# Performance work log

Measured on AMD Instinct MI355X. Metric: run time of the kernel, lower is better.

## Reference

```python
import jax, jax.numpy as jnp
import numpy as np

CODEBOOK_SIZE = 1024
LATENT_DIM = 64
BETA = 0.25      # commitment_beta
DECAY = 0.99     # ema_decay
EPS = 1e-5       # ema_eps
DIVERSITY_W = 1.0


def _hadamard(n):
    # Sylvester construction (n must be a power of 2)
    H = np.array([[1.0]], dtype=np.float32)
    while H.shape[0] < n:
        H = np.block([[H, H], [H, -H]])
    return H.astype(np.float32)


def setup_inputs() -> dict:
    key = jax.random.key(0)
    k1, k2, k3 = jax.random.split(key, 3)
    B, C, H, W = 32, LATENT_DIM, 32, 32
    x = jax.random.normal(k1, (B, C, H, W), dtype=jnp.float32)
    embedding_weight = jax.random.normal(k2, (CODEBOOK_SIZE, LATENT_DIM), dtype=jnp.float32)
    rotation_matrix = jnp.asarray(_hadamard(LATENT_DIM))
    ema_w = jax.random.normal(k3, (CODEBOOK_SIZE, LATENT_DIM), dtype=jnp.float32)
    ema_cluster_size = jnp.ones((CODEBOOK_SIZE,), dtype=jnp.float32)
    return {"x": x, "embedding_weight": embedding_weight,
            "rotation_matrix": rotation_matrix, "ema_w": ema_w,
            "ema_cluster_size": ema_cluster_size}


def reference(x, embedding_weight, rotation_matrix, ema_w, ema_cluster_size):
    B, C, H, W = x.shape
    K, D = embedding_weight.shape
    N = B * H * W
    sg = jax.lax.stop_gradient

    # flatten channel-last, rotate
    xf = jnp.transpose(x, (0, 2, 3, 1)).reshape(N, D)      # [N, D]
    xr = xf @ rotation_matrix                               # [N, D]

    # pairwise squared distances to codebook + argmin
    dist = (jnp.sum(xr * xr, axis=-1, keepdims=True)
            + jnp.sum(embedding_weight * embedding_weight, axis=-1)[None, :]
            - 2.0 * (xr @ embedding_weight.T))              # [N, K]
    idx = jnp.argmin(dist, axis=-1)                         # [N]

    # one-hot scatter equivalents (counts / dw) done with index scatter-add
    counts = jnp.zeros((K,), x.dtype).at[idx].add(1.0)      # encodings.sum(0)
    quant = embedding_weight[idx]                           # [N, D]
    # NOTE: original code views (B*H*W, C) row-major directly as (B, C, H, W)
    quant_out = quant.reshape(B, C, H, W)

    # EMA codebook update (training=True path)
    cs = ema_cluster_size * DECAY + (1.0 - DECAY) * counts
    n = jnp.sum(cs)
    cs = (cs + EPS) / (n + K * EPS) * n
    dw = jnp.zeros((K, D), x.dtype).at[idx].add(xr)         # encodings.T @ xr
    new_ema_w = ema_w * DECAY + (1.0 - DECAY) * dw
    new_embedding = new_ema_w / cs[:, None]

    commitment_loss = BETA * jnp.mean((sg(quant_out) - x) ** 2)
    codebook_loss = jnp.mean((quant_out - sg(x)) ** 2)

    # diversity: mean over ALL (i, j) pairs of ||e_i - xr_j||^2 (original
    # broadcasts (N,1,D) vs (N,D) -> (N,N,D)); identical closed form:
    e = new_embedding[idx]                                  # [N, D]
    diversity_loss = DIVERSITY_W * (jnp.mean(jnp.sum(e * e, axis=-1))
                                    + jnp.mean(jnp.sum(xr * xr, axis=-1))
                                    - 2.0 * jnp.dot(jnp.mean(e, axis=0), jnp.mean(xr, axis=0)))

    avg_probs = counts / N
    perplexity = jnp.exp(-jnp.sum(avg_probs * jnp.log(avg_probs + 1e-10)))

    quant_st = x + sg(quant_out - x)                        # straight-through
    return (quant_st, codebook_loss, commitment_loss, diversity_loss,
            perplexity, idx, cs, new_ema_w, new_embedding)
```

## Files before the change

### kernel.cpp

```cpp
#include <hip/hip_runtime.h>
#include <math.h>

#define NTOK 32768
#define KCB  1024
#define DIM  64
#define THETA 0.02f

typedef __attribute__((ext_vector_type(8))) short short8;
typedef __attribute__((ext_vector_type(4))) float f32x4;
#define MFMA __builtin_amdgcn_mfma_f32_16x16x32_bf16
#define ALOAD(p) __hip_atomic_load((p), __ATOMIC_RELAXED, __HIP_MEMORY_SCOPE_AGENT)

#define WS_XR      0
#define WS_ENORM   2097152
#define WS_EH      2098176
#define WS_EL      2130944
#define WS_COUNTS  2163712
#define WS_CS      2164736
#define WS_XRSUM   2165760
#define WS_ESUM    2166272
#define WS_SCALREP 2166784
#define WS_FLAGCNT 2166912
#define WS_IDX     2166928
#define WS_FLAG    2199696

#define O_Q    0
#define O_CB   2097152
#define O_CM   2097153
#define O_DV   2097154
#define O_PP   2097155
#define O_IDX  2097156
#define O_CS   2129924
#define O_EW   2130948
#define O_EMB  2196484

__device__ __forceinline__ void hilo(float v, unsigned &h, unsigned &l)
{
    unsigned b  = __float_as_uint(v);
    unsigned hb = (b + 0x7FFFu + ((b >> 16) & 1u)) & 0xFFFF0000u;
    float lof   = v - __uint_as_float(hb);
    unsigned lb = __float_as_uint(lof);
    l = (lb + 0x7FFFu + ((lb >> 16) & 1u)) >> 16;
    h = hb >> 16;
}

__global__ __launch_bounds__(256) void k_rotate_enorm(const float* __restrict__ x,
    const float* __restrict__ E, float* __restrict__ xr, float* __restrict__ enorm,
    unsigned short* __restrict__ eh, unsigned short* __restrict__ el,
    float* __restrict__ counts, int* __restrict__ flagc,
    float* __restrict__ e_sum, float* __restrict__ xr_sum,
    float* __restrict__ scalrep)
{
    int tid = threadIdx.x;
    if (blockIdx.x >= 512) {
        int b = (int)blockIdx.x - 512;
        counts[(b << 8) + tid] = 0.f;
        if (b == 0) {
            if (tid < 16) flagc[tid] = 0;
            if (tid < 128) scalrep[tid] = 0.f;
        } else if (b == 1) {
            e_sum[tid] = 0.f; e_sum[256 + tid] = 0.f;
        } else if (b == 2) {
            xr_sum[tid] = 0.f; xr_sum[256 + tid] = 0.f;
        }
        int k = (b << 8) + tid;
        const float* ep = E + ((size_t)k << 6);
        unsigned* ehw = (unsigned*)eh + (k << 5);
        unsigned* elw = (unsigned*)el + (k << 5);
        float s = 0.f;
        #pragma unroll
        for (int q = 0; q < 32; ++q) {
            float v0 = ep[2*q], v1 = ep[2*q+1];
            s = fmaf(v0, v0, s); s = fmaf(v1, v1, s);
            unsigned h0, l0, h1, l1;
            hilo(v0, h0, l0);
            hilo(v1, h1, l1);
            ehw[q] = h0 | (h1 << 16);
            elw[q] = l0 | (l1 << 16);
        }
        enorm[k] = s;
        return;
    }
    __shared__ float xt[64 * 65];
    int p  = blockIdx.x >> 4;
    int s0 = ((int)blockIdx.x & 15) << 6;

    {
        const float4* x4 = (const float4*)x;
        #pragma unroll
        for (int pass = 0; pass < 4; ++pass) {
            int q = (pass << 8) + tid;
            int c = q >> 4, col = (q & 15) << 2;
            float4 v = x4[(p << 14) + (c << 8) + (s0 >> 2) + (col >> 2)];
            float* dst = xt + c * 65 + col;
            dst[0] = v.x; dst[1] = v.y; dst[2] = v.z; dst[3] = v.w;
        }
    }
    __syncthreads();

    int lane = tid & 63, w = tid >> 6;
    #pragma unroll
    for (int i = 0; i < 4; ++i) {
        int sl = (w << 4) + (i << 2);
        const float* src = xt + lane * 65 + sl;
        float4 v = make_float4(src[0], src[1], src[2], src[3]);
        #pragma unroll
        for (int s = 1; s <= 32; s <<= 1) {
            float sgn = (lane & s) ? -1.f : 1.f;
            float ox = __shfl_xor(v.x, s);
            float oy = __shfl_xor(v.y, s);
            float oz = __shfl_xor(v.z, s);
            float ow = __shfl_xor(v.w, s);
            v.x = fmaf(sgn, v.x, ox);
            v.y = fmaf(sgn, v.y, oy);
            v.z = fmaf(sgn, v.z, oz);
            v.w = fmaf(sgn, v.w, ow);
        }
        int t0 = ((int)blockIdx.x << 6) + sl;
        float* dst = xr + ((size_t)t0 << 6) + lane;
        dst[0]   = v.x;
        dst[64]  = v.y;
        dst[128] = v.z;
        dst[192] = v.w;
    }
}

__global__ __launch_bounds__(256, 4) void k_argmin(const float* __restrict__ xr,
    const unsigned short* __restrict__ eh, const unsigned short* __restrict__ el,
    const float* __restrict__ enorm, int* __restrict__ idxw,
    float* __restrict__ out_idx, float* __restrict__ counts,
    int* __restrict__ flag)
{
    __shared__ uint4 ehs[1024];
    __shared__ uint4 els[1024];
    __shared__ float ens[128];
    __shared__ float m_b1[32], m_b2[32];
    __shared__ int   m_id[32];
    int tid = threadIdx.x;
    int lane = tid & 63, w = tid >> 6;
    int ts = w >> 1, kh = w & 1;
    int tx = lane & 15, gq = lane >> 4;
    int tokbase = ((int)blockIdx.x << 5) + (ts << 4);

    short8 ah0, al0, ah1, al1;
    {
        const float* xp = xr + ((size_t)(tokbase + tx) << 6) + (gq << 3);
        float4 xa = *(const float4*)(xp);
        float4 xb = *(const float4*)(xp + 4);
        float4 xc = *(const float4*)(xp + 32);
        float4 xd = *(const float4*)(xp + 36);
        float a0v[8] = {xa.x,xa.y,xa.z,xa.w,xb.x,xb.y,xb.z,xb.w};
        float a1v[8] = {xc.x,xc.y,xc.z,xc.w,xd.x,xd.y,xd.z,xd.w};
        #pragma unroll
        for (int j = 0; j < 8; ++j) {
            unsigned h, l;
            hilo(a0v[j], h, l);
            ah0[j] = (short)h; al0[j] = (short)l;
            hilo(a1v[j], h, l);
            ah1[j] = (short)h; al1[j] = (short)l;
        }
    }

    float b1[4], b2[4]; int idx[4];
    #pragma unroll
    for (int r = 0; r < 4; ++r) { b1[r] = 3.4e38f; b2[r] = 3.4e38f; idx[r] = 0; }

    int swz0 = gq ^ (tx & 7);
    int swz1 = (4 + gq) ^ (tx & 7);
    const f32x4 z4 = {0.f, 0.f, 0.f, 0.f};

    for (int ch = 0; ch < 8; ++ch) {
        int c0 = ch << 7;
        __syncthreads();
        {
            const uint4* ghs = (const uint4*)eh + ((size_t)c0 << 3);
            const uint4* gls = (const uint4*)el + ((size_t)c0 << 3);
            #pragma unroll
            for (int i = 0; i < 4; ++i) {
                int u = (i << 8) + tid;
                int rr = u >> 3, bb = u & 7;
                int bs = bb ^ (rr & 7);
                ehs[(rr << 3) + bs] = ghs[u];
                els[(rr << 3) + bs] = gls[u];
            }
            if (tid < 128) ens[tid] = enorm[c0 + tid];
        }
        __syncthreads();

        #pragma unroll
        for (int s = 0; s < 4; ++s) {
            int rbase = (kh << 6) + (s << 4) + tx;
            short8 bh0 = ((const short8*)ehs)[(rbase << 3) + swz0];
            short8 bh1 = ((const short8*)ehs)[(rbase << 3) + swz1];
            short8 bl0 = ((const short8*)els)[(rbase << 3) + swz0];
            short8 bl1 = ((const short8*)els)[(rbase << 3) + swz1];

            f32x4 a0 = MFMA(ah0, bh0, z4, 0, 0, 0);
            a0 = MFMA(ah0, bl0, a0, 0, 0, 0);
            a0 = MFMA(al0, bh0, a0, 0, 0, 0);
            f32x4 a1 = MFMA(ah1, bh1, z4, 0, 0, 0);
            a1 = MFMA(ah1, bl1, a1, 0, 0, 0);
            a1 = MFMA(al1, bh1, a1, 0, 0, 0);

            float en = ens[rbase];
            int kk = c0 + rbase;
            #pragma unroll
            for (int r = 0; r < 4; ++r) {
                float sv = fmaf(-2.f, a0[r], fmaf(-2.f, a1[r], en));
                float mx = fmaxf(sv, b1[r]);
                b2[r] = fminf(b2[r], mx);
                bool t = sv < b1[r];
                idx[r] = t ? kk : idx[r];
                b1[r] = fminf(b1[r], sv);
            }
        }
    }

    float v1f[4], v2f[4]; int idf[4];
    #pragma unroll
    for (int r = 0; r < 4; ++r) {
        float v1 = b1[r], v2 = b2[r]; int id = idx[r];
        #pragma unroll
        for (int m = 1; m <= 8; m <<= 1) {
            float o1 = __shfl_xor(v1, m);
            float o2 = __shfl_xor(v2, m);
            int   oi = __shfl_xor(id, m);
            float nb2 = fminf(fminf(v2, o2), fmaxf(v1, o1));
            bool t = (o1 < v1) || (o1 == v1 && oi < id);
            v1 = t ? o1 : v1;
            id = t ? oi : id;
            v2 = nb2;
        }
        v1f[r] = v1; v2f[r] = v2; idf[r] = id;
    }

    int tl = (ts << 4) + (gq << 2);
    if (kh == 1 && tx == 0) {
        #pragma unroll
        for (int r = 0; r < 4; ++r) {
            m_b1[tl + r] = v1f[r];
            m_b2[tl + r] = v2f[r];
            m_id[tl + r] = idf[r];
        }
    }
    __syncthreads();
    if (kh == 0 && tx == 0) {
        #pragma unroll
        for (int r = 0; r < 4; ++r) {
            float o1 = m_b1[tl + r], o2 = m_b2[tl + r];
            int   oi = m_id[tl + r];
            float v1 = v1f[r]; int id = idf[r];
            float b2m = fminf(fminf(v2f[r], o2), fmaxf(v1, o1));
            bool t = (o1 < v1) || (o1 == v1 && oi < id);
            float v1m = t ? o1 : v1;
            int   idm = t ? oi : id;
            int tok = tokbase + (gq << 2) + r;
            idxw[tok] = idm;
            out_idx[tok] = (float)idm;
            atomicAdd(&counts[idm], 1.f);
            flag[tok] = (b2m - v1m < THETA) ? 1 : 0;
        }
    }
}

__global__ __launch_bounds__(256) void k_fixupquant_ema(const float* __restrict__ x,
    const float* __restrict__ xr, const float* __restrict__ E,
    const float* __restrict__ enorm, const float* __restrict__ ecs,
    const int* __restrict__ flag, int* __restrict__ idxw,
    float* __restrict__ out_idx, float* __restrict__ counts,
    float* __restrict__ out_cs, float* __restrict__ csw,
    int* __restrict__ done_ctr, float* __restrict__ outq,
    float* __restrict__ scalrep)
{
    __shared__ int lidx[32];
    __shared__ unsigned fmask;
    __shared__ float wr[4], wn[4];
    int tid = threadIdx.x;
    int lane = tid & 63, w = tid >> 6;
    int n0 = (int)blockIdx.x << 5;

    int fl = 0;
    if (tid < 32) {
        lidx[tid] = idxw[n0 + tid];
        fl = flag[n0 + tid];
    }
    unsigned long long bal = __ballot(fl != 0);
    if (tid == 0) fmask = (unsigned)bal;
    __syncthreads();

    unsigned msk = fmask;
    int widx = 0;
    while (msk) {
        int src = __ffs(msk) - 1; msk &= msk - 1;
        if ((widx++ & 3) != w) continue;
        int tok = n0 + src;
        const float4* xp = (const float4*)(xr + ((size_t)tok << 6));
        float4 xa[16];
        #pragma unroll
        for (int q = 0; q < 16; ++q) xa[q] = xp[q];
        float best = 3.4e38f; int bidx = 0;
        for (int c = 0; c < 16; ++c) {
            int k = (c << 6) + lane;
            const float4* epp = (const float4*)(E + ((size_t)k << 6));
            float d = 0.f;
            #pragma unroll
            for (int q = 0; q < 16; ++q) {
                float4 e = epp[q];
                d = fmaf(xa[q].x, e.x, d);
                d = fmaf(xa[q].y, e.y, d);
                d = fmaf(xa[q].z, e.z, d);
                d = fmaf(xa[q].w, e.w, d);
            }
            float sv = fmaf(-2.f, d, enorm[k]);
            if (sv < best) { best = sv; bidx = k; }
        }
        #pragma unroll
        for (int m = 1; m <= 32; m <<= 1) {
            float ov = __shfl_xor(best, m);
            int   oi = __shfl_xor(bidx, m);
            if (ov < best || (ov == best && oi < bidx)) { best = ov; bidx = oi; }
        }
        if (lane == 0) {
            int old = lidx[src];
            if (old != bidx) {
                atomicAdd(&counts[old], -1.f);
                atomicAdd(&counts[bidx], 1.f);
                lidx[src] = bidx;
                idxw[tok] = bidx;
                out_idx[tok] = (float)bidx;
            }
        }
    }
    __syncthreads();

    int f40 = (int)blockIdx.x << 9;
    float sq = 0.f, xn = 0.f;
    #pragma unroll
    for (int it = 0; it < 2; ++it) {
        int q = (it << 8) + tid;
        int kk = lidx[q >> 4];
        int d4 = q & 15;
        float4 xv = ((const float4*)x)[f40 + q];
        float4 ev = ((const float4*)E)[(kk << 4) + d4];
        float dx = ev.x - xv.x, dy = ev.y - xv.y, dz = ev.z - xv.z, dw_ = ev.w - xv.w;
        ((float4*)outq)[f40 + q] = make_float4(xv.x + dx, xv.y + dy, xv.z + dz, xv.w + dw_);
        sq += dx*dx + dy*dy + dz*dz + dw_*dw_;
        xn += xv.x*xv.x + xv.y*xv.y + xv.z*xv.z + xv.w*xv.w;
    }
    #pragma unroll
    for (int m = 32; m >= 1; m >>= 1) { sq += __shfl_xor(sq, m); xn += __shfl_xor(xn, m); }
    if (lane == 0) { wr[w] = sq; wn[w] = xn; }
    __syncthreads();
    if (tid == 0) {
        int rep = ((int)blockIdx.x & 7) << 4;
        atomicAdd(&scalrep[rep + 0], wr[0] + wr[1] + wr[2] + wr[3]);
        atomicAdd(&scalrep[rep + 1], wn[0] + wn[1] + wn[2] + wn[3]);
    }

    __shared__ int ticket;
    __syncthreads();
    if (tid == 0) ticket = atomicAdd(done_ctr, 1);
    __syncthreads();
    if (ticket != 1023) return;

    __shared__ float wsum2[4];
    __shared__ float nss;
    float cs4[4];
    float csum = 0.f;
    #pragma unroll
    for (int j = 0; j < 4; ++j) {
        int kk = (tid << 2) + j;
        float c = ALOAD(&counts[kk]);
        float cs = ecs[kk] * 0.99f + 0.01f * c;
        cs4[j] = cs;
        csum += cs;
    }
    float v = csum;
    #pragma unroll
    for (int m = 32; m >= 1; m >>= 1) v += __shfl_xor(v, m);
    if (lane == 0) wsum2[w] = v;
    __syncthreads();
    if (tid == 0) nss = wsum2[0] + wsum2[1] + wsum2[2] + wsum2[3];
    __syncthreads();
    float nn = nss;
    #pragma unroll
    for (int j = 0; j < 4; ++j) {
        int kk = (tid << 2) + j;
        float csf = (cs4[j] + 1e-5f) / (nn + 1024.f * 1e-5f) * nn;
        out_cs[kk] = csf;
        csw[kk] = csf;
    }
}

__global__ __launch_bounds__(256) void k_dwemb_final(const float* __restrict__ xr,
    const int* __restrict__ idxw, const float* __restrict__ counts,
    const float* __restrict__ csw, const float* __restrict__ emaw,
    float* __restrict__ out_ew, float* __restrict__ out_emb,
    float* __restrict__ e_sum, float* __restrict__ scalrep,
    float* __restrict__ xr_sum, float* __restrict__ out,
    int* __restrict__ done_ctr)
{
    __shared__ float part[3][64];
    __shared__ int   lst[2048];
    __shared__ int   lcnt;
    int k = blockIdx.x;
    int tid = threadIdx.x;
    int w = tid >> 6, d = tid & 63;

    if (tid == 0) lcnt = 0;
    __syncthreads();
    for (int t = tid; t < NTOK; t += 256) {
        if (idxw[t] == k) {
            int p = atomicAdd(&lcnt, 1);
            if (p < 2048) lst[p] = t;
        }
    }
    __syncthreads();
    int cnt = lcnt;

    float sum = 0.f;
    for (int j = w; j < cnt; j += 4) {
        int tok = lst[j];
        sum += xr[((size_t)tok << 6) + d];
    }
    if (w) part[w - 1][d] = sum;
    __syncthreads();
    if (w == 0) {
        float dw = sum + part[0][d] + part[1][d] + part[2][d];
        int i = (k << 6) + d;
        float nw = emaw[i] * 0.99f + 0.01f * dw;
        out_ew[i] = nw;
        float emb = nw / csw[k];
        out_emb[i] = emb;
        if (cnt > 0) {
            int rep = (k & 7) << 6;
            atomicAdd(&xr_sum[rep + d], dw);
            float c = (float)cnt;
            atomicAdd(&e_sum[rep + d], c * emb);
            float t2 = c * emb * emb;
            #pragma unroll
            for (int m = 32; m >= 1; m >>= 1) t2 += __shfl_xor(t2, m);
            if (d == 0) atomicAdd(&scalrep[((k & 7) << 4) + 2], t2);
        }
    }

    __shared__ int ticket;
    __syncthreads();
    if (tid == 0) ticket = atomicAdd(done_ctr, 1);
    __syncthreads();
    if (ticket != 1023) return;

    __shared__ float wt[4], wd[4];
    float tt = 0.f;
    #pragma unroll
    for (int j = 0; j < 4; ++j) {
        float aa = ALOAD(&counts[(tid << 2) + j]) * (1.f / 32768.f);
        tt += aa * logf(aa + 1e-10f);
    }
    float dc = 0.f;
    if (tid < 64) {
        float xs8 = 0.f, es8 = 0.f;
        #pragma unroll
        for (int r2 = 0; r2 < 8; ++r2) {
            xs8 += ALOAD(&xr_sum[(r2 << 6) + tid]);
            es8 += ALOAD(&e_sum[(r2 << 6) + tid]);
        }
        dc = es8 * xs8;
    }
    #pragma unroll
    for (int m = 32; m >= 1; m >>= 1) { tt += __shfl_xor(tt, m); dc += __shfl_xor(dc, m); }
    if ((tid & 63) == 0) { wt[w] = tt; wd[w] = dc; }
    __syncthreads();
    if (tid == 0) {
        float S = wt[0] + wt[1] + wt[2] + wt[3];
        float Dt = wd[0] + wd[1] + wd[2] + wd[3];
        float sqs = 0.f, xns = 0.f, s2s = 0.f;
        #pragma unroll
        for (int r2 = 0; r2 < 8; ++r2) {
            sqs += scalrep[(r2 << 4) + 0];
            xns += scalrep[(r2 << 4) + 1];
            s2s += ALOAD(&scalrep[(r2 << 4) + 2]);
        }
        float cb = sqs * (1.f / 2097152.f);
        out[O_CB] = cb;
        out[O_CM] = 0.25f * cb;
        float inv = 1.f / 32768.f;
        out[O_DV] = s2s * inv + 64.f * xns * inv - 2.f * (Dt * inv * inv);
        out[O_PP] = expf(-S);
    }
}

extern "C" void kernel_launch(void* const* d_in, const int* in_sizes, int n_in,
                              void* d_out, int out_size, void* d_ws, size_t ws_size,
                              hipStream_t stream)
{
    const float* x    = (const float*)d_in[0];
    const float* E    = (const float*)d_in[1];
    const float* emaw = (const float*)d_in[3];
    const float* ecs  = (const float*)d_in[4];
    float* out = (float*)d_out;
    float* ws  = (float*)d_ws;
    int* flagc = (int*)(ws + WS_FLAGCNT);

    hipLaunchKernelGGL(k_rotate_enorm, dim3(516), dim3(256), 0, stream,
                       x, E, ws + WS_XR, ws + WS_ENORM,
                       (unsigned short*)(ws + WS_EH), (unsigned short*)(ws + WS_EL),
                       ws + WS_COUNTS, flagc,
                       ws + WS_ESUM, ws + WS_XRSUM, ws + WS_SCALREP);
    hipLaunchKernelGGL(k_argmin, dim3(1024), dim3(256), 0, stream,
                       ws + WS_XR, (const unsigned short*)(ws + WS_EH),
                       (const unsigned short*)(ws + WS_EL), ws + WS_ENORM,
                       (int*)(ws + WS_IDX), out + O_IDX, ws + WS_COUNTS,
                       (int*)(ws + WS_FLAG));
    hipLaunchKernelGGL(k_fixupquant_ema, dim3(1024), dim3(256), 0, stream,
                       x, ws + WS_XR, E, ws + WS_ENORM, ecs,
                       (const int*)(ws + WS_FLAG), (int*)(ws + WS_IDX),
                       out + O_IDX, ws + WS_COUNTS, out + O_CS, ws + WS_CS,
                       flagc + 1, out + O_Q, ws + WS_SCALREP);
    hipLaunchKernelGGL(k_dwemb_final, dim3(1024), dim3(256), 0, stream,
                       ws + WS_XR, (const int*)(ws + WS_IDX), ws + WS_COUNTS,
                       ws + WS_CS, emaw, out + O_EW, out + O_EMB, ws + WS_ESUM,
                       ws + WS_SCALREP, ws + WS_XRSUM, out, flagc + 2);
}
```

Measured before the change: 124.4 us.

## Replace per-code full token scan with counting-sort bucket lists plus correction log

Instead of each of 1024 blocks scanning all 32768 indices to find its tokens, the last argmin block computes an exclusive prefix sum of counts, and the fixup kernel scatters token ids into per-code buckets. The dw kernel then reads only its own segment and applies a small log of reassigned tokens (old/new code) from the fixup pass. This removes the quadratic-ish index scan but adds global atomics for bucket placement and a serial correction loop per block, which could become costly if many tokens get reassigned.

```diff
diff --git a/kernel.cpp b/kernel.cpp
--- a/kernel.cpp
+++ b/kernel.cpp
@@ -5,6 +5,7 @@
 #define KCB  1024
 #define DIM  64
 #define THETA 0.02f
+#define MAXCORR 8192
 
 typedef __attribute__((ext_vector_type(8))) short short8;
 typedef __attribute__((ext_vector_type(4))) float f32x4;
@@ -23,6 +24,11 @@
 #define WS_FLAGCNT 2166912
 #define WS_IDX     2166928
 #define WS_FLAG    2199696
+#define WS_SORT    2232464
+#define WS_OFF     2265232
+#define WS_CUR     2266256
+#define WS_PCNT    2267280
+#define WS_CORR    2268304
 
 #define O_Q    0
 #define O_CB   2097152
@@ -129,7 +135,8 @@
     const unsigned short* __restrict__ eh, const unsigned short* __restrict__ el,
     const float* __restrict__ enorm, int* __restrict__ idxw,
     float* __restrict__ out_idx, float* __restrict__ counts,
-    int* __restrict__ flag)
+    int* __restrict__ flag, int* __restrict__ off, int* __restrict__ cur,
+    int* __restrict__ pcnt, int* __restrict__ done_ctr)
 {
     __shared__ uint4 ehs[1024];
     __shared__ uint4 els[1024];
@@ -261,14 +268,54 @@
             flag[tok] = (b2m - v1m < THETA) ? 1 : 0;
         }
     }
+
+    __shared__ int ticket;
+    __syncthreads();
+    if (tid == 0) ticket = atomicAdd(done_ctr, 1);
+    __syncthreads();
+    if (ticket != 1023) return;
+
+    __shared__ int wcnt2[4], woff2[4];
+    int ci4[4]; int s = 0;
+    #pragma unroll
+    for (int j = 0; j < 4; ++j) {
+        int kk = (tid << 2) + j;
+        ci4[j] = (int)ALOAD(&counts[kk]);
+        s += ci4[j];
+    }
+    int sc = s;
+    #pragma unroll
+    for (int o = 1; o < 64; o <<= 1) {
+        int u = __shfl_up(sc, o);
+        if (lane >= o) sc += u;
+    }
+    if (lane == 63) wcnt2[w] = sc;
+    __syncthreads();
+    if (tid == 0) {
+        int run = 0;
+        #pragma unroll
+        for (int i = 0; i < 4; ++i) { woff2[i] = run; run += wcnt2[i]; }
+    }
+    __syncthreads();
+    int run = woff2[w] + (sc - s);
+    #pragma unroll
+    for (int j = 0; j < 4; ++j) {
+        int kk = (tid << 2) + j;
+        off[kk] = run;
+        cur[kk] = run;
+        pcnt[kk] = ci4[j];
+        run += ci4[j];
+    }
 }
 
-__global__ __launch_bounds__(256) void k_fixupquant_ema(const float* __restrict__ x,
+__global__ __launch_bounds__(256) void k_fixupquant_cs(const float* __restrict__ x,
     const float* __restrict__ xr, const float* __restrict__ E,
     const float* __restrict__ enorm, const float* __restrict__ ecs,
     const int* __restrict__ flag, int* __restrict__ idxw,
     float* __restrict__ out_idx, float* __restrict__ counts,
     float* __restrict__ out_cs, float* __restrict__ csw,
+    int* __restrict__ cur, int* __restrict__ sorted,
+    int* __restrict__ corrctr, int* __restrict__ corr,
     int* __restrict__ done_ctr, float* __restrict__ outq,
     float* __restrict__ scalrep)
 {
@@ -281,8 +328,11 @@
 
     int fl = 0;
     if (tid < 32) {
-        lidx[tid] = idxw[n0 + tid];
+        int k = idxw[n0 + tid];
+        lidx[tid] = k;
         fl = flag[n0 + tid];
+        int pos = atomicAdd(&cur[k], 1);
+        sorted[pos] = n0 + tid;
     }
     unsigned long long bal = __ballot(fl != 0);
     if (tid == 0) fmask = (unsigned)bal;
@@ -328,6 +378,11 @@
                 lidx[src] = bidx;
                 idxw[tok] = bidx;
                 out_idx[tok] = (float)bidx;
+                int p = atomicAdd(corrctr, 1);
+                if (p < MAXCORR) {
+                    corr[2*p]   = tok;
+                    corr[2*p+1] = (old << 10) | bidx;
+                }
             }
         }
     }
@@ -393,40 +448,50 @@
 }
 
 __global__ __launch_bounds__(256) void k_dwemb_final(const float* __restrict__ xr,
-    const int* __restrict__ idxw, const float* __restrict__ counts,
+    const int* __restrict__ sorted, const int* __restrict__ off,
+    const int* __restrict__ pcnt, const float* __restrict__ counts,
     const float* __restrict__ csw, const float* __restrict__ emaw,
+    const int* __restrict__ corrctr, const int* __restrict__ corr,
     float* __restrict__ out_ew, float* __restrict__ out_emb,
     float* __restrict__ e_sum, float* __restrict__ scalrep,
     float* __restrict__ xr_sum, float* __restrict__ out,
     int* __restrict__ done_ctr)
 {
     __shared__ float part[3][64];
-    __shared__ int   lst[2048];
-    __shared__ int   lcnt;
+    __shared__ int   seg[2048];
     int k = blockIdx.x;
     int tid = threadIdx.x;
     int w = tid >> 6, d = tid & 63;
-
-    if (tid == 0) lcnt = 0;
-    __syncthreads();
-    for (int t = tid; t < NTOK; t += 256) {
-        if (idxw[t] == k) {
-            int p = atomicAdd(&lcnt, 1);
-            if (p < 2048) lst[p] = t;
-        }
-    }
-    __syncthreads();
-    int cnt = lcnt;
+    int a = off[k];
+    int cntp = pcnt[k];
+    int end = a + cntp;
 
     float sum = 0.f;
-    for (int j = w; j < cnt; j += 4) {
-        int tok = lst[j];
-        sum += xr[((size_t)tok << 6) + d];
-    }
+    for (int base = a; base < end; base += 2048) {
+        int clen = min(2048, end - base);
+        __syncthreads();
+        for (int t = tid; t < clen; t += 256) seg[t] = sorted[base + t];
+        __syncthreads();
+        #pragma unroll 2
+        for (int j = w; j < clen; j += 4) {
+            int tok = seg[j];
+            sum += xr[((size_t)tok << 6) + d];
+        }
+    }
+    __syncthreads();
     if (w) part[w - 1][d] = sum;
     __syncthreads();
     if (w == 0) {
         float dw = sum + part[0][d] + part[1][d] + part[2][d];
+        int nc = min(corrctr[0], MAXCORR);
+        for (int i = 0; i < nc; ++i) {
+            int tok = corr[2*i];
+            int on  = corr[2*i+1];
+            int ok = on >> 10, nk = on & 1023;
+            if (ok == k) dw -= xr[((size_t)tok << 6) + d];
+            if (nk == k) dw += xr[((size_t)tok << 6) + d];
+        }
+        int cnt = (int)counts[k];
         int i = (k << 6) + d;
         float nw = emaw[i] * 0.99f + 0.01f * dw;
         out_ew[i] = nw;
@@ -511,14 +576,20 @@
                        ws + WS_XR, (const unsigned short*)(ws + WS_EH),
                        (const unsigned short*)(ws + WS_EL), ws + WS_ENORM,
                        (int*)(ws + WS_IDX), out + O_IDX, ws + WS_COUNTS,
-                       (int*)(ws + WS_FLAG));
-    hipLaunchKernelGGL(k_fixupquant_ema, dim3(1024), dim3(256), 0, stream,
+                       (int*)(ws + WS_FLAG), (int*)(ws + WS_OFF),
+                       (int*)(ws + WS_CUR), (int*)(ws + WS_PCNT), flagc + 1);
+    hipLaunchKernelGGL(k_fixupquant_cs, dim3(1024), dim3(256), 0, stream,
                        x, ws + WS_XR, E, ws + WS_ENORM, ecs,
                        (const int*)(ws + WS_FLAG), (int*)(ws + WS_IDX),
                        out + O_IDX, ws + WS_COUNTS, out + O_CS, ws + WS_CS,
-                       flagc + 1, out + O_Q, ws + WS_SCALREP);
+                       (int*)(ws + WS_CUR), (int*)(ws + WS_SORT),
+                       flagc, (int*)(ws + WS_CORR), flagc + 2,
+                       out + O_Q, ws + WS_SCALREP);
     hipLaunchKernelGGL(k_dwemb_final, dim3(1024), dim3(256), 0, stream,
-                       ws + WS_XR, (const int*)(ws + WS_IDX), ws + WS_COUNTS,
-                       ws + WS_CS, emaw, out + O_EW, out + O_EMB, ws + WS_ESUM,
-                       ws + WS_SCALREP, ws + WS_XRSUM, out, flagc + 2);
+                       ws + WS_XR, (const int*)(ws + WS_SORT),
+                       (const int*)(ws + WS_OFF), (const int*)(ws + WS_PCNT),
+                       ws + WS_COUNTS, ws + WS_CS, emaw,
+                       (const int*)flagc, (const int*)(ws + WS_CORR),
+                       out + O_EW, out + O_EMB, ws + WS_ESUM,
+                       ws + WS_SCALREP, ws + WS_XRSUM, out, flagc + 3);
 }
```

Result: faster. 99.68 us (median of 2 runs) (-19.8%).
